# Kernel tuning notes

Measured on AMD Instinct MI355X. Metric: run time of the kernel, lower is better.

Reference implementation:

```python
import jax, jax.numpy as jnp
import numpy as np

B, N, D, F, L, R = 16, 1024, 256, 128, 2, 2


def setup_inputs() -> dict:
    key = jax.random.key(0)
    ks = jax.random.split(key, 12)
    s = 0.05
    return {
        "node_embed": jax.random.normal(ks[0], (B, N, D), jnp.float32),
        "input_x": jax.random.normal(ks[1], (B, F), jnp.float32),
        "adj": jax.random.randint(ks[2], (R, B, N, N), 0, 2, jnp.int32),
        "WQi_w": jax.random.normal(ks[3], (L, F, F), jnp.float32) * s,
        "WQi_b": jnp.zeros((L, F), jnp.float32),
        "WQ_w": jax.random.normal(ks[4], (L, D + F, D), jnp.float32) * s,
        "WQ_b": jnp.zeros((L, D), jnp.float32),
        "WK_w": jax.random.normal(ks[5], (L, R, D + F, D), jnp.float32) * s,
        "WK_b": jnp.zeros((L, R, D), jnp.float32),
        "WV_w": jax.random.normal(ks[6], (L, R, D + F, D), jnp.float32) * s,
        "WV_b": jnp.zeros((L, R, D), jnp.float32),
        "WF_w": jax.random.normal(ks[7], (L, R * D, D), jnp.float32) * s,
        "WF_b": jnp.zeros((L, D), jnp.float32),
        "ln_g": jnp.ones((L, D), jnp.float32),
        "ln_b": jnp.zeros((L, D), jnp.float32),
    }


def _layer_norm(x, g, b, eps=1e-5):
    mu = jnp.mean(x, axis=-1, keepdims=True)
    var = jnp.var(x, axis=-1, keepdims=True)
    return (x - mu) * jax.lax.rsqrt(var + eps) * g + b


def reference(node_embed, input_x, adj, WQi_w, WQi_b, WQ_w, WQ_b,
              WK_w, WK_b, WV_w, WV_b, WF_w, WF_b, ln_g, ln_b):
    scale = 1.0 / (D ** 0.5)
    h = node_embed
    for l in range(L):
        # input feature projection, broadcast over nodes
        x1 = input_x @ WQi_w[l] + WQi_b[l]              # (B, F)
        x1 = jnp.broadcast_to(x1[:, None, :], (h.shape[0], h.shape[1], F))
        qc = jnp.concatenate([h, x1], axis=-1)          # (B, N, D+F)
        q = qc @ WQ_w[l] + WQ_b[l]                      # (B, N, D)
        outs = []
        for r in range(R):
            k = qc @ WK_w[l, r] + WK_b[l, r]            # (B, N, D)
            v = qc @ WV_w[l, r] + WV_b[l, r]            # (B, N, D)
            scores = jnp.einsum('bnd,bmd->bnm', q, k) * scale
            scores = jnp.where(adj[r] == 0, -1e9, scores)
            alpha = jax.nn.softmax(scores, axis=-1)
            outs.append(jnp.einsum('bnm,bmd->bnd', alpha, v))
        h_concat = jnp.concatenate(outs, axis=-1)       # (B, N, R*D)
        h_fused = jax.nn.relu(h_concat @ WF_w[l] + WF_b[l])
        h = _layer_norm(h + h_fused, ln_g[l], ln_b[l])
    return h
```

## Files before the change

### kernel.cpp

```cpp
#include <hip/hip_runtime.h>
#include <hip/hip_bf16.h>

#define BB 16
#define NN 1024
#define DD 256
#define FF_ 128
#define LL 2
#define RR 2
#define DF 384
#define MM (BB*NN)
#define NPROJ 1280
#define PK 768

typedef __attribute__((ext_vector_type(8))) short s16x8;
typedef __attribute__((ext_vector_type(4))) float f32x4;
typedef __attribute__((ext_vector_type(16))) float f32x16;
typedef __attribute__((ext_vector_type(4))) unsigned int u32x4;
typedef __attribute__((ext_vector_type(4))) unsigned short us16x4;

__device__ __forceinline__ unsigned short f2bf(float f){
  unsigned u = __builtin_bit_cast(unsigned, f);
  u += 0x7fff + ((u >> 16) & 1);
  return (unsigned short)(u >> 16);
}

__device__ __forceinline__ void gload16(const void* g, void* l){
  __builtin_amdgcn_global_load_lds(
      (const __attribute__((address_space(1))) unsigned int*)g,
      (__attribute__((address_space(3))) unsigned int*)l, 16, 0, 0);
}

#define MFMA16(a,b,c) __builtin_amdgcn_mfma_f32_16x16x32_bf16((a),(b),(c),0,0,0)
#define MFMA32(a,b,c) __builtin_amdgcn_mfma_f32_32x32x16_bf16((a),(b),(c),0,0,0)

__global__ __launch_bounds__(256) void pack_adj(const int* __restrict__ adj,
                                                unsigned long long* __restrict__ bits){
  int w = threadIdx.x >> 6, lane = threadIdx.x & 63;
  size_t row = (size_t)blockIdx.x * 4 + w;
  const int* a = adj + row * NN;
  unsigned long long* brow = bits + row * 16;
  #pragma unroll
  for (int j = 0; j < 16; ++j){
    unsigned long long m = __ballot(a[j*64 + lane] != 0);
    if (lane == 0) brow[j] = m;
  }
}

#define PREP_WT   3840
#define PREP_WTF  1024
#define PREP_BALL 10
#define PREP_X1   16
#define PREP_H    2048
#define PREP_TOT  (PREP_WT+PREP_WTF+PREP_BALL+PREP_X1+PREP_H)

__global__ __launch_bounds__(256) void prep(
    const float* __restrict__ node, const float* __restrict__ inx,
    const float* __restrict__ WQi_w, const float* __restrict__ WQi_b,
    const float* __restrict__ WQ_w, const float* __restrict__ WK_w,
    const float* __restrict__ WV_w, const float* __restrict__ WQ_b,
    const float* __restrict__ WK_b, const float* __restrict__ WV_b,
    const float* __restrict__ WF_w,
    unsigned short* __restrict__ wtall, unsigned short* __restrict__ wtf,
    float* __restrict__ ball, unsigned short* __restrict__ x1bf,
    unsigned short* __restrict__ hbf){
  int bid = blockIdx.x, t = threadIdx.x;
  if (bid < PREP_WT){
    int o = bid*256 + t;
    int l = o / (NPROJ*DF); int oo = o - l*(NPROJ*DF);
    int n = oo / DF, k = oo - n*DF;
    const float* WQ = WQ_w + (size_t)l*DF*256;
    const float* WK = WK_w + (size_t)l*RR*DF*256;
    const float* WV = WV_w + (size_t)l*RR*DF*256;
    float v;
    if (n < 256)      v = WQ[(size_t)k*256 + n];
    else if (n < 768) v = WK[(size_t)((n-256)>>8)*(DF*256) + (size_t)k*256 + ((n-256)&255)];
    else              v = WV[(size_t)((n-768)>>8)*(DF*256) + (size_t)k*256 + ((n-768)&255)];
    wtall[o] = f2bf(v);
  } else if (bid < PREP_WT + PREP_WTF){
    int o = (bid - PREP_WT)*256 + t;
    int l = o >> 17; int oo = o & 131071;
    int n = oo >> 9, k = oo & 511;
    wtf[o] = f2bf(WF_w[(size_t)l*512*256 + (size_t)k*256 + n]);
  } else if (bid < PREP_WT + PREP_WTF + PREP_BALL){
    int o = (bid - PREP_WT - PREP_WTF)*256 + t;
    if (o < 2*NPROJ){
      int l = o / NPROJ, n = o - l*NPROJ;
      float v = (n < 256) ? WQ_b[l*256 + n]
              : (n < 768) ? WK_b[(size_t)l*512 + (n-256)]
                          : WV_b[(size_t)l*512 + (n-768)];
      ball[o] = v;
    }
  } else if (bid < PREP_WT + PREP_WTF + PREP_BALL + PREP_X1){
    int o = (bid - PREP_WT - PREP_WTF - PREP_BALL)*256 + t;
    int l = o >> 11, bj = o & 2047;
    int b = bj >> 7, j = bj & 127;
    const float* w = WQi_w + (size_t)l*FF_*FF_;
    float s = WQi_b[l*FF_ + j];
    for (int i = 0; i < FF_; ++i) s += inx[b*FF_ + i] * w[i*FF_ + j];
    x1bf[o] = f2bf(s);
  } else {
    int o = (bid - (PREP_TOT - PREP_H))*256 + t;
    const float4* src = (const float4*)node + (size_t)o*2;
    float4 a = src[0], c = src[1];
    uint4 pk;
    pk.x = (unsigned)f2bf(a.x) | ((unsigned)f2bf(a.y) << 16);
    pk.y = (unsigned)f2bf(a.z) | ((unsigned)f2bf(a.w) << 16);
    pk.z = (unsigned)f2bf(c.x) | ((unsigned)f2bf(c.y) << 16);
    pk.w = (unsigned)f2bf(c.z) | ((unsigned)f2bf(c.w) << 16);
    *(uint4*)(hbf + (size_t)o*8) = pk;
  }
}

__global__ __launch_bounds__(256) void gemm_big(const unsigned short* __restrict__ hbf,
    const unsigned short* __restrict__ x1l, const unsigned short* __restrict__ Wt,
    const float* __restrict__ bias, unsigned short* __restrict__ POUT,
    unsigned short* __restrict__ vtall){
  __shared__ unsigned short As[2][128*32];
  __shared__ unsigned short Bs[2][128*32];
  int t = threadIdx.x, lane = t & 63, w = t >> 6;
  int wr = w >> 1, wc = w & 1, l15 = lane & 15, lhi = lane >> 4;
  int bm = blockIdx.x, bn = blockIdx.y, bb = bm >> 3;
  f32x4 acc[4][4];
  #pragma unroll
  for (int m = 0; m < 4; ++m)
    #pragma unroll
    for (int n = 0; n < 4; ++n) acc[m][n] = (f32x4){0.f,0.f,0.f,0.f};

  auto STAGE = [&](int bi, int kk){
    #pragma unroll
    for (int i = 0; i < 2; ++i){
      int base = w*2048 + i*1024;
      int off = base + lane*16;
      int row = off >> 6, cb = off & 63;
      const char* asrc = (kk < 8)
        ? (const char*)hbf + ((size_t)(bm*128 + row)*256 + kk*32)*2 + cb
        : (const char*)x1l + ((size_t)bb*128 + (kk-8)*32)*2 + cb;
      gload16(asrc, (char*)As[bi] + base);
      gload16((const char*)Wt + ((size_t)(bn*128 + row)*DF + kk*32)*2 + cb,
              (char*)Bs[bi] + base);
    }
  };

  STAGE(0, 0);
  __syncthreads();
  for (int kk = 0; kk < 12; ++kk){
    int cur = kk & 1;
    if (kk + 1 < 12) STAGE(cur ^ 1, kk + 1);
    s16x8 af[4], bfr[4];
    #pragma unroll
    for (int m = 0; m < 4; ++m) af[m]  = *(const s16x8*)&As[cur][(wr*64 + m*16 + l15)*32 + lhi*8];
    #pragma unroll
    for (int n = 0; n < 4; ++n) bfr[n] = *(const s16x8*)&Bs[cur][(wc*64 + n*16 + l15)*32 + lhi*8];
    __builtin_amdgcn_s_setprio(1);
    #pragma unroll
    for (int m = 0; m < 4; ++m)
      #pragma unroll
      for (int n = 0; n < 4; ++n)
        acc[m][n] = MFMA16(af[m], bfr[n], acc[m][n]);
    __builtin_amdgcn_s_setprio(0);
    __syncthreads();
  }

  if (bn < 6){
    #pragma unroll
    for (int n = 0; n < 4; ++n){
      int gn = bn*128 + wc*64 + n*16 + l15;
      float bv = bias[gn];
      #pragma unroll
      for (int m = 0; m < 4; ++m){
        int gm = bm*128 + wr*64 + m*16 + lhi*4;
        #pragma unroll
        for (int i = 0; i < 4; ++i)
          POUT[(size_t)(gm + i)*PK + gn] = f2bf(acc[m][n][i] + bv);
      }
    }
  } else {
    #pragma unroll
    for (int n = 0; n < 4; ++n){
      int gn = bn*128 + wc*64 + n*16 + l15;
      float bv = bias[gn];
      int rv = gn - 768;
      int r = rv >> 8, d = rv & 255;
      #pragma unroll
      for (int m = 0; m < 4; ++m){
        int mb = (bm & 7)*128 + wr*64 + m*16 + lhi*4;
        us16x4 pk;
        #pragma unroll
        for (int i = 0; i < 4; ++i) pk[i] = f2bf(acc[m][n][i] + bv);
        *(us16x4*)(vtall + ((size_t)((r*16 + bb)*256 + d))*NN + mb) = pk;
      }
    }
  }
}

__global__ __launch_bounds__(512, 2) void attn4(const unsigned short* __restrict__ P,
    const unsigned short* __restrict__ VT, const unsigned long long* __restrict__ bits,
    unsigned short* __restrict__ hc){
  __shared__ unsigned short Kt[64*256];
  __shared__ unsigned short Vt[256*64];
  int t = threadIdx.x, lane = t & 63, w = t >> 6;
  int h = lane >> 5, l31 = lane & 31;
  int qsub = w >> 1, dh = w & 1;
  int F = blockIdx.x;
  int xcd = F & 7, j = F >> 3;
  int qt = j & 7;
  int gidx = xcd*4 + (j >> 3);
  int b = gidx & 15, r = gidx >> 4;
  const float C = 0.09016844f;

  size_t kcol = 256 + (size_t)r*256;
  const unsigned short* Vb = VT + ((size_t)(r*16 + b))*256*NN;

  int qrow = qt*128 + qsub*32 + l31;
  s16x8 qf[16];
  {
    const unsigned short* qp = P + ((size_t)(b*NN + qrow))*PK + h*8;
    #pragma unroll
    for (int d_ = 0; d_ < 16; ++d_) qf[d_] = *(const s16x8*)(qp + d_*16);
  }

  f32x16 acc[4];
  #pragma unroll
  for (int dt = 0; dt < 4; ++dt)
    #pragma unroll
    for (int i = 0; i < 16; ++i) acc[dt][i] = 0.f;
  float mrow = -3e38f, lrow = 0.f;
  const unsigned long long* bitp = bits + ((size_t)(r*BB + b)*NN + qrow)*16;

  for (int kt = 0; kt < 16; ++kt){
    __syncthreads();
    #pragma unroll
    for (int i = 0; i < 4; ++i){
      int base = w*4096 + i*1024;
      int off = base + lane*16;
      int row = off >> 9, cb = off & 511;
      int scb = cb ^ ((row & 7) << 4);
      gload16((const char*)P + ((size_t)(b*NN + kt*64 + row)*PK + kcol)*2 + scb,
              (char*)Kt + base);
    }
    #pragma unroll
    for (int i = 0; i < 4; ++i){
      int base = w*4096 + i*1024;
      int off = base + lane*16;
      int row = off >> 7, cb = off & 127;
      int scb = cb ^ ((row & 7) << 4);
      gload16((const char*)Vb + ((size_t)row*NN + kt*64)*2 + scb,
              (char*)Vt + base);
    }
    __syncthreads();

    f32x16 st[2];
    #pragma unroll
    for (int s = 0; s < 2; ++s){
      #pragma unroll
      for (int i = 0; i < 16; ++i) st[s][i] = 0.f;
      int krow = s*32 + l31;
      int swz = (krow & 7) << 4;
      #pragma unroll
      for (int d_ = 0; d_ < 16; ++d_){
        s16x8 kf = *(const s16x8*)((const char*)Kt + krow*512 + ((d_*32 + h*16) ^ swz));
        st[s] = MFMA32(kf, qf[d_], st[s]);
      }
    }

    unsigned long long mwv = bitp[kt];
    float ev[2][16];
    float tm = -3e38f;
    #pragma unroll
    for (int s = 0; s < 2; ++s)
      #pragma unroll
      for (int rr = 0; rr < 16; ++rr){
        int kb = s*32 + (rr & 3) + 8*(rr >> 2) + 4*h;
        float sval = st[s][rr] * C;
        sval = ((mwv >> kb) & 1ULL) ? sval : -1.443e9f;
        ev[s][rr] = sval;
        tm = fmaxf(tm, sval);
      }
    tm = fmaxf(tm, __shfl_xor(tm, 32));
    bool need = tm > mrow + 11.6f;
    if (__any(need)){
      float f = need ? exp2f(mrow - tm) : 1.f;
      if (need) mrow = tm;
      lrow *= f;
      #pragma unroll
      for (int rr = 0; rr < 16; ++rr){
        float fr = __shfl(f, (rr & 3) + 8*(rr >> 2) + 4*h);
        acc[0][rr] *= fr; acc[1][rr] *= fr; acc[2][rr] *= fr; acc[3][rr] *= fr;
      }
    }
    float rs = 0.f;
    #pragma unroll
    for (int s = 0; s < 2; ++s)
      #pragma unroll
      for (int rr = 0; rr < 16; ++rr){
        float e = exp2f(ev[s][rr] - mrow);
        ev[s][rr] = e;
        rs += e;
      }
    rs += __shfl_xor(rs, 32);
    lrow += rs;

    unsigned Pm[2][4][2];
    #pragma unroll
    for (int s = 0; s < 2; ++s)
      #pragma unroll
      for (int m = 0; m < 4; ++m)
        #pragma unroll
        for (int c = 0; c < 2; ++c)
          Pm[s][m][c] = (unsigned)f2bf(ev[s][4*m + 2*c])
                      | ((unsigned)f2bf(ev[s][4*m + 2*c + 1]) << 16);

    s16x8 pa[4];
    #pragma unroll
    for (int ks = 0; ks < 4; ++ks){
      const int s = ks >> 1, idx = ks & 1;
      unsigned own0 = h ? Pm[s][2*idx+1][0] : Pm[s][2*idx][0];
      unsigned own1 = h ? Pm[s][2*idx+1][1] : Pm[s][2*idx][1];
      unsigned snd0 = h ? Pm[s][2*idx][0]   : Pm[s][2*idx+1][0];
      unsigned snd1 = h ? Pm[s][2*idx][1]   : Pm[s][2*idx+1][1];
      unsigned rx0 = (unsigned)__shfl_xor((int)snd0, 32);
      unsigned rx1 = (unsigned)__shfl_xor((int)snd1, 32);
      u32x4 pv;
      pv[0] = h ? rx0 : own0;
      pv[1] = h ? rx1 : own1;
      pv[2] = h ? own0 : rx0;
      pv[3] = h ? own1 : rx1;
      pa[ks] = __builtin_bit_cast(s16x8, pv);
    }

    #pragma unroll
    for (int dt = 0; dt < 4; ++dt){
      int vrow = dh*128 + dt*32 + l31;
      int swz = (vrow & 7) << 4;
      #pragma unroll
      for (int ks = 0; ks < 4; ++ks){
        s16x8 vf = *(const s16x8*)((const char*)Vt + vrow*128 + ((ks*32 + h*16) ^ swz));
        acc[dt] = MFMA32(pa[ks], vf, acc[dt]);
      }
    }
  }

  float linv = 1.f / lrow;
  #pragma unroll
  for (int rr = 0; rr < 16; ++rr){
    int rowo = (rr & 3) + 8*(rr >> 2) + 4*h;
    float ir = __shfl(linv, rowo);
    int q = qt*128 + qsub*32 + rowo;
    unsigned short* hrow = hc + ((size_t)(b*NN + q))*(RR*DD) + r*DD + dh*128 + l31;
    #pragma unroll
    for (int dt = 0; dt < 4; ++dt)
      hrow[dt*32] = f2bf(acc[dt][rr] * ir);
  }
}

__global__ __launch_bounds__(256) void gemm_ff(const unsigned short* __restrict__ A,
    const unsigned short* __restrict__ Wt, const float* __restrict__ bias,
    float* __restrict__ out){
  __shared__ unsigned short As[2][128*32];
  __shared__ unsigned short Bs[2][128*32];
  int t = threadIdx.x, lane = t & 63, w = t >> 6;
  int wr = w >> 1, wc = w & 1, l15 = lane & 15, lhi = lane >> 4;
  int bm = blockIdx.x, bn = blockIdx.y;
  f32x4 acc[4][4];
  #pragma unroll
  for (int m = 0; m < 4; ++m)
    #pragma unroll
    for (int n = 0; n < 4; ++n) acc[m][n] = (f32x4){0.f,0.f,0.f,0.f};

  auto STAGE = [&](int bi, int kk){
    #pragma unroll
    for (int i = 0; i < 2; ++i){
      int base = w*2048 + i*1024;
      int off = base + lane*16;
      int row = off >> 6, cb = off & 63;
      gload16((const char*)A  + ((size_t)(bm*128 + row)*512 + kk*32)*2 + cb,
              (char*)As[bi] + base);
      gload16((const char*)Wt + ((size_t)(bn*128 + row)*512 + kk*32)*2 + cb,
              (char*)Bs[bi] + base);
    }
  };

  STAGE(0, 0);
  __syncthreads();
  for (int kk = 0; kk < 16; ++kk){
    int cur = kk & 1;
    if (kk + 1 < 16) STAGE(cur ^ 1, kk + 1);
    s16x8 af[4], bfr[4];
    #pragma unroll
    for (int m = 0; m < 4; ++m) af[m]  = *(const s16x8*)&As[cur][(wr*64 + m*16 + l15)*32 + lhi*8];
    #pragma unroll
    for (int n = 0; n < 4; ++n) bfr[n] = *(const s16x8*)&Bs[cur][(wc*64 + n*16 + l15)*32 + lhi*8];
    __builtin_amdgcn_s_setprio(1);
    #pragma unroll
    for (int m = 0; m < 4; ++m)
      #pragma unroll
      for (int n = 0; n < 4; ++n)
        acc[m][n] = MFMA16(af[m], bfr[n], acc[m][n]);
    __builtin_amdgcn_s_setprio(0);
    __syncthreads();
  }

  #pragma unroll
  for (int n = 0; n < 4; ++n){
    int gn = bn*128 + wc*64 + n*16 + l15;
    float bv = bias[gn];
    #pragma unroll
    for (int m = 0; m < 4; ++m){
      int gm = bm*128 + wr*64 + m*16 + lhi*4;
      #pragma unroll
      for (int i = 0; i < 4; ++i)
        out[(size_t)(gm + i)*DD + gn] = acc[m][n][i] + bv;
    }
  }
}

template<int WRITEH>
__global__ __launch_bounds__(256) void ln_res2(const float* __restrict__ ff,
    const float* __restrict__ hin, const float* __restrict__ g,
    const float* __restrict__ bv, float* __restrict__ hout,
    unsigned short* __restrict__ hbf){
  int w = threadIdx.x >> 6, lane = threadIdx.x & 63;
  size_t row = (size_t)blockIdx.x * 4 + w;
  f32x4 fv = *(const f32x4*)(ff  + row*DD + lane*4);
  f32x4 hv = *(const f32x4*)(hin + row*DD + lane*4);
  float x[4], s = 0.f, ss = 0.f;
  #pragma unroll
  for (int j = 0; j < 4; ++j){ x[j] = fmaxf(fv[j], 0.f) + hv[j]; s += x[j]; ss += x[j]*x[j]; }
  #pragma unroll
  for (int xm = 1; xm < 64; xm <<= 1){ s += __shfl_xor(s, xm); ss += __shfl_xor(ss, xm); }
  float mu = s * (1.f/256.f);
  float var = ss * (1.f/256.f) - mu*mu;
  float rstd = rsqrtf(var + 1e-5f);
  f32x4 o;
  #pragma unroll
  for (int j = 0; j < 4; ++j){ int c = lane*4 + j; o[j] = (x[j]-mu)*rstd*g[c] + bv[c]; }
  *(f32x4*)(hout + row*DD + lane*4) = o;
  if (WRITEH){
    uint2 pv;
    pv.x = (unsigned)f2bf(o[0]) | ((unsigned)f2bf(o[1]) << 16);
    pv.y = (unsigned)f2bf(o[2]) | ((unsigned)f2bf(o[3]) << 16);
    *(uint2*)(hbf + row*DD + lane*4) = pv;
  }
}

extern "C" void kernel_launch(void* const* d_in, const int* in_sizes, int n_in,
                              void* d_out, int out_size, void* d_ws, size_t ws_size,
                              hipStream_t stream){
  (void)in_sizes; (void)n_in; (void)out_size; (void)ws_size;
  const float* node  = (const float*)d_in[0];
  const float* inx   = (const float*)d_in[1];
  const int*   adj   = (const int*)d_in[2];
  const float* WQi_w = (const float*)d_in[3];
  const float* WQi_b = (const float*)d_in[4];
  const float* WQ_w  = (const float*)d_in[5];
  const float* WQ_b  = (const float*)d_in[6];
  const float* WK_w  = (const float*)d_in[7];
  const float* WK_b  = (const float*)d_in[8];
  const float* WV_w  = (const float*)d_in[9];
  const float* WV_b  = (const float*)d_in[10];
  const float* WF_w  = (const float*)d_in[11];
  const float* WF_b  = (const float*)d_in[12];
  const float* ln_g  = (const float*)d_in[13];
  const float* ln_b  = (const float*)d_in[14];
  float* hout = (float*)d_out;

  char* wsp = (char*)d_ws;
  auto alloc = [&](size_t n){ char* p = wsp; wsp += (n + 255) & ~(size_t)255; return p; };
  unsigned long long* bits = (unsigned long long*)alloc((size_t)RR*BB*NN*16*8);
  unsigned short* wtall = (unsigned short*)alloc((size_t)2*NPROJ*DF*2);
  unsigned short* wtf   = (unsigned short*)alloc((size_t)2*DD*512*2);
  float*          ball  = (float*)alloc((size_t)2*NPROJ*4);
  unsigned short* x1bf  = (unsigned short*)alloc((size_t)2*BB*FF_*2);
  unsigned short* hbf   = (unsigned short*)alloc((size_t)MM*DD*2);
  unsigned short* POUT  = (unsigned short*)alloc((size_t)MM*PK*2);
  unsigned short* vtall = (unsigned short*)alloc((size_t)RR*BB*DD*NN*2);
  unsigned short* hc    = (unsigned short*)alloc((size_t)MM*512*2);
  float*          ffo   = (float*)alloc((size_t)MM*DD*4);

  pack_adj<<<RR*BB*NN/4, 256, 0, stream>>>(adj, bits);
  prep<<<PREP_TOT, 256, 0, stream>>>(node, inx, WQi_w, WQi_b, WQ_w, WK_w, WV_w,
                                     WQ_b, WK_b, WV_b, WF_w,
                                     wtall, wtf, ball, x1bf, hbf);

  for (int l = 0; l < LL; ++l){
    gemm_big<<<dim3(128,10), 256, 0, stream>>>(hbf, x1bf + (size_t)l*BB*FF_,
        wtall + (size_t)l*NPROJ*DF, ball + (size_t)l*NPROJ, POUT, vtall);

    attn4<<<256, 512, 0, stream>>>(POUT, vtall, bits, hc);

    gemm_ff<<<dim3(128,2), 256, 0, stream>>>(hc, wtf + (size_t)l*DD*512, WF_b + l*DD, ffo);

    if (l == 0) ln_res2<1><<<MM/4, 256, 0, stream>>>(ffo, node, ln_g, ln_b, hout, hbf);
    else        ln_res2<0><<<MM/4, 256, 0, stream>>>(ffo, (const float*)hout,
                                                     ln_g + DD, ln_b + DD, hout, nullptr);
  }
}
```

Before: 325.9 us.

## Rework attention kernel with double-buffered K/V tiles and full-D waves

Replaces attn4 with attn5, which uses 256 threads where each wave handles 32 query rows across the full 256-wide head dimension, so P@V needs no split across waves. K/V tiles are double-buffered in 128KB of LDS with async global-to-LDS loads, and the next tile is prefetched while the current one is computed. Softmax now runs per 32-key half, using hardware bf16 pack conversion and a per-thread rescale instead of shuffles. Output is staged through LDS so stores to global memory are coalesced. The cost is one block per CU and more accumulator registers (8 f32x16 per lane), which lowers occupancy.

```diff
diff --git a/kernel.cpp b/kernel.cpp
--- a/kernel.cpp
+++ b/kernel.cpp
@@ -15,6 +15,7 @@
 typedef __attribute__((ext_vector_type(8))) short s16x8;
 typedef __attribute__((ext_vector_type(4))) float f32x4;
 typedef __attribute__((ext_vector_type(16))) float f32x16;
+typedef __attribute__((ext_vector_type(2))) unsigned int u32x2;
 typedef __attribute__((ext_vector_type(4))) unsigned int u32x4;
 typedef __attribute__((ext_vector_type(4))) unsigned short us16x4;
 
@@ -193,14 +194,13 @@
   }
 }
 
-__global__ __launch_bounds__(512, 2) void attn4(const unsigned short* __restrict__ P,
+__global__ __launch_bounds__(256, 1) void attn5(const unsigned short* __restrict__ P,
     const unsigned short* __restrict__ VT, const unsigned long long* __restrict__ bits,
     unsigned short* __restrict__ hc){
-  __shared__ unsigned short Kt[64*256];
-  __shared__ unsigned short Vt[256*64];
+  __shared__ char smem[131072];
+
   int t = threadIdx.x, lane = t & 63, w = t >> 6;
   int h = lane >> 5, l31 = lane & 31;
-  int qsub = w >> 1, dh = w & 1;
   int F = blockIdx.x;
   int xcd = F & 7, j = F >> 3;
   int qt = j & 7;
@@ -211,7 +211,8 @@
   size_t kcol = 256 + (size_t)r*256;
   const unsigned short* Vb = VT + ((size_t)(r*16 + b))*256*NN;
 
-  int qrow = qt*128 + qsub*32 + l31;
+  int qrow = qt*128 + w*32 + l31;
+
   s16x8 qf[16];
   {
     const unsigned short* qp = P + ((size_t)(b*NN + qrow))*PK + h*8;
@@ -219,137 +220,161 @@
     for (int d_ = 0; d_ < 16; ++d_) qf[d_] = *(const s16x8*)(qp + d_*16);
   }
 
-  f32x16 acc[4];
-  #pragma unroll
-  for (int dt = 0; dt < 4; ++dt)
+  f32x16 acc[8];
+  #pragma unroll
+  for (int dt = 0; dt < 8; ++dt)
     #pragma unroll
     for (int i = 0; i < 16; ++i) acc[dt][i] = 0.f;
   float mrow = -3e38f, lrow = 0.f;
   const unsigned long long* bitp = bits + ((size_t)(r*BB + b)*NN + qrow)*16;
 
-  for (int kt = 0; kt < 16; ++kt){
-    __syncthreads();
-    #pragma unroll
-    for (int i = 0; i < 4; ++i){
-      int base = w*4096 + i*1024;
+  auto STAGE = [&](int bi, int kt){
+    char* Kd = smem + bi*32768;
+    char* Vd = smem + 65536 + bi*32768;
+    #pragma unroll
+    for (int i = 0; i < 8; ++i){
+      int base = w*8192 + i*1024;
       int off = base + lane*16;
       int row = off >> 9, cb = off & 511;
       int scb = cb ^ ((row & 7) << 4);
       gload16((const char*)P + ((size_t)(b*NN + kt*64 + row)*PK + kcol)*2 + scb,
-              (char*)Kt + base);
-    }
-    #pragma unroll
-    for (int i = 0; i < 4; ++i){
-      int base = w*4096 + i*1024;
+              Kd + base);
+    }
+    #pragma unroll
+    for (int i = 0; i < 8; ++i){
+      int base = w*8192 + i*1024;
       int off = base + lane*16;
       int row = off >> 7, cb = off & 127;
       int scb = cb ^ ((row & 7) << 4);
       gload16((const char*)Vb + ((size_t)row*NN + kt*64)*2 + scb,
-              (char*)Vt + base);
-    }
-    __syncthreads();
-
-    f32x16 st[2];
+              Vd + base);
+    }
+  };
+
+  STAGE(0, 0);
+
+  for (int kt = 0; kt < 16; ++kt){
+    __builtin_amdgcn_s_barrier();
+    unsigned long long mwv = bitp[kt];
+    if (kt + 1 < 16){
+      STAGE((kt+1)&1, kt+1);
+      asm volatile("s_waitcnt vmcnt(16)" ::: "memory");
+    } else {
+      asm volatile("s_waitcnt vmcnt(0)" ::: "memory");
+    }
+    __builtin_amdgcn_s_barrier();
+    __builtin_amdgcn_sched_barrier(0);
+
+    const char* Kcur = smem + (kt & 1)*32768;
+    const char* Vcur = smem + 65536 + (kt & 1)*32768;
+
     #pragma unroll
     for (int s = 0; s < 2; ++s){
-      #pragma unroll
-      for (int i = 0; i < 16; ++i) st[s][i] = 0.f;
+      f32x16 st;
+      #pragma unroll
+      for (int i = 0; i < 16; ++i) st[i] = 0.f;
       int krow = s*32 + l31;
-      int swz = (krow & 7) << 4;
+      int swzk = (krow & 7) << 4;
+      const char* kbase = Kcur + krow*512;
       #pragma unroll
       for (int d_ = 0; d_ < 16; ++d_){
-        s16x8 kf = *(const s16x8*)((const char*)Kt + krow*512 + ((d_*32 + h*16) ^ swz));
-        st[s] = MFMA32(kf, qf[d_], st[s]);
-      }
-    }
-
-    unsigned long long mwv = bitp[kt];
-    float ev[2][16];
-    float tm = -3e38f;
-    #pragma unroll
-    for (int s = 0; s < 2; ++s)
+        s16x8 kf = *(const s16x8*)(kbase + ((d_*32 + h*16) ^ swzk));
+        st = MFMA32(kf, qf[d_], st);
+      }
+
+      unsigned mw = (unsigned)(mwv >> (s*32));
+      float tm = -3e38f;
       #pragma unroll
       for (int rr = 0; rr < 16; ++rr){
-        int kb = s*32 + (rr & 3) + 8*(rr >> 2) + 4*h;
-        float sval = st[s][rr] * C;
-        sval = ((mwv >> kb) & 1ULL) ? sval : -1.443e9f;
-        ev[s][rr] = sval;
-        tm = fmaxf(tm, sval);
-      }
-    tm = fmaxf(tm, __shfl_xor(tm, 32));
-    bool need = tm > mrow + 11.6f;
-    if (__any(need)){
-      float f = need ? exp2f(mrow - tm) : 1.f;
-      if (need) mrow = tm;
-      lrow *= f;
+        int kb = (rr & 3) + 8*(rr >> 2) + 4*h;
+        float sv = st[rr] * C;
+        sv = ((mw >> kb) & 1u) ? sv : -1.443e9f;
+        st[rr] = sv;
+        tm = fmaxf(tm, sv);
+      }
+      tm = fmaxf(tm, __shfl_xor(tm, 32));
+      if (tm > mrow + 10.f){
+        float f = exp2f(mrow - tm);
+        mrow = tm;
+        lrow *= f;
+        #pragma unroll
+        for (int dt = 0; dt < 8; ++dt)
+          #pragma unroll
+          for (int i = 0; i < 16; ++i) acc[dt][i] *= f;
+      }
+      float rs = 0.f;
       #pragma unroll
       for (int rr = 0; rr < 16; ++rr){
-        float fr = __shfl(f, (rr & 3) + 8*(rr >> 2) + 4*h);
-        acc[0][rr] *= fr; acc[1][rr] *= fr; acc[2][rr] *= fr; acc[3][rr] *= fr;
-      }
-    }
-    float rs = 0.f;
-    #pragma unroll
-    for (int s = 0; s < 2; ++s)
-      #pragma unroll
-      for (int rr = 0; rr < 16; ++rr){
-        float e = exp2f(ev[s][rr] - mrow);
-        ev[s][rr] = e;
+        float e = exp2f(st[rr] - mrow);
+        st[rr] = e;
         rs += e;
       }
-    rs += __shfl_xor(rs, 32);
-    lrow += rs;
-
-    unsigned Pm[2][4][2];
-    #pragma unroll
-    for (int s = 0; s < 2; ++s)
-      #pragma unroll
-      for (int m = 0; m < 4; ++m)
-        #pragma unroll
-        for (int c = 0; c < 2; ++c)
-          Pm[s][m][c] = (unsigned)f2bf(ev[s][4*m + 2*c])
-                      | ((unsigned)f2bf(ev[s][4*m + 2*c + 1]) << 16);
-
-    s16x8 pa[4];
-    #pragma unroll
-    for (int ks = 0; ks < 4; ++ks){
-      const int s = ks >> 1, idx = ks & 1;
-      unsigned own0 = h ? Pm[s][2*idx+1][0] : Pm[s][2*idx][0];
-      unsigned own1 = h ? Pm[s][2*idx+1][1] : Pm[s][2*idx][1];
-      unsigned snd0 = h ? Pm[s][2*idx][0]   : Pm[s][2*idx+1][0];
-      unsigned snd1 = h ? Pm[s][2*idx][1]   : Pm[s][2*idx+1][1];
-      unsigned rx0 = (unsigned)__shfl_xor((int)snd0, 32);
-      unsigned rx1 = (unsigned)__shfl_xor((int)snd1, 32);
-      u32x4 pv;
-      pv[0] = h ? rx0 : own0;
-      pv[1] = h ? rx1 : own1;
-      pv[2] = h ? own0 : rx0;
-      pv[3] = h ? own1 : rx1;
-      pa[ks] = __builtin_bit_cast(s16x8, pv);
-    }
-
-    #pragma unroll
-    for (int dt = 0; dt < 4; ++dt){
-      int vrow = dh*128 + dt*32 + l31;
-      int swz = (vrow & 7) << 4;
-      #pragma unroll
-      for (int ks = 0; ks < 4; ++ks){
-        s16x8 vf = *(const s16x8*)((const char*)Vt + vrow*128 + ((ks*32 + h*16) ^ swz));
-        acc[dt] = MFMA32(pa[ks], vf, acc[dt]);
-      }
-    }
-  }
-
-  float linv = 1.f / lrow;
-  #pragma unroll
-  for (int rr = 0; rr < 16; ++rr){
-    int rowo = (rr & 3) + 8*(rr >> 2) + 4*h;
-    float ir = __shfl(linv, rowo);
-    int q = qt*128 + qsub*32 + rowo;
-    unsigned short* hrow = hc + ((size_t)(b*NN + q))*(RR*DD) + r*DD + dh*128 + l31;
-    #pragma unroll
-    for (int dt = 0; dt < 4; ++dt)
-      hrow[dt*32] = f2bf(acc[dt][rr] * ir);
+      rs += __shfl_xor(rs, 32);
+      lrow += rs;
+
+      unsigned pk[8];
+      #pragma unroll
+      for (int p = 0; p < 8; ++p){
+        unsigned rpk;
+        float lo = st[p*2], hi = st[p*2+1];
+        asm("v_cvt_pk_bf16_f32 %0, %1, %2" : "=v"(rpk) : "v"(lo), "v"(hi));
+        pk[p] = rpk;
+      }
+      unsigned sA = h ? pk[0] : pk[2], sB = h ? pk[1] : pk[3];
+      unsigned sC = h ? pk[4] : pk[6], sD = h ? pk[5] : pk[7];
+      unsigned rxA = (unsigned)__shfl_xor((int)sA, 32);
+      unsigned rxB = (unsigned)__shfl_xor((int)sB, 32);
+      unsigned rxC = (unsigned)__shfl_xor((int)sC, 32);
+      unsigned rxD = (unsigned)__shfl_xor((int)sD, 32);
+      u32x4 pv0, pv1;
+      pv0[0] = h ? rxA : pk[0]; pv0[1] = h ? rxB : pk[1];
+      pv0[2] = h ? pk[2] : rxA; pv0[3] = h ? pk[3] : rxB;
+      pv1[0] = h ? rxC : pk[4]; pv1[1] = h ? rxD : pk[5];
+      pv1[2] = h ? pk[6] : rxC; pv1[3] = h ? pk[7] : rxD;
+      s16x8 pa0 = __builtin_bit_cast(s16x8, pv0);
+      s16x8 pa1 = __builtin_bit_cast(s16x8, pv1);
+
+      #pragma unroll
+      for (int dt = 0; dt < 8; ++dt){
+        int vrow = dt*32 + l31;
+        int swzv = (vrow & 7) << 4;
+        const char* vbase = Vcur + vrow*128;
+        s16x8 vf0 = *(const s16x8*)(vbase + (((2*s)*32 + h*16) ^ swzv));
+        acc[dt] = MFMA32(vf0, pa0, acc[dt]);
+        s16x8 vf1 = *(const s16x8*)(vbase + (((2*s+1)*32 + h*16) ^ swzv));
+        acc[dt] = MFMA32(vf1, pa1, acc[dt]);
+      }
+    }
+  }
+
+  __builtin_amdgcn_s_barrier();
+  float inv = 1.f / lrow;
+  unsigned short* Ob = (unsigned short*)smem;
+  int qloc = w*32 + l31;
+  #pragma unroll
+  for (int dt = 0; dt < 8; ++dt){
+    #pragma unroll
+    for (int g = 0; g < 4; ++g){
+      float a0 = acc[dt][g*4+0]*inv, a1 = acc[dt][g*4+1]*inv;
+      float a2 = acc[dt][g*4+2]*inv, a3 = acc[dt][g*4+3]*inv;
+      unsigned r0, r1;
+      asm("v_cvt_pk_bf16_f32 %0, %1, %2" : "=v"(r0) : "v"(a0), "v"(a1));
+      asm("v_cvt_pk_bf16_f32 %0, %1, %2" : "=v"(r1) : "v"(a2), "v"(a3));
+      int d = dt*32 + 8*g + 4*h;
+      int byteoff = qloc*512 + ((d*2) ^ ((qloc & 7) << 4));
+      u32x2 pv; pv[0] = r0; pv[1] = r1;
+      *(u32x2*)((char*)Ob + byteoff) = pv;
+    }
+  }
+  __builtin_amdgcn_s_barrier();
+  #pragma unroll
+  for (int it = 0; it < 16; ++it){
+    int off = (it*256 + t) * 16;
+    int row = off >> 9, cb = off & 511;
+    int scb = cb ^ ((row & 7) << 4);
+    u32x4 v = *(const u32x4*)((char*)Ob + row*512 + scb);
+    int q = qt*128 + row;
+    *(u32x4*)((char*)hc + (((size_t)(b*NN + q))*512 + r*256 + (cb >> 1))*2) = v;
   }
 }
 
@@ -486,7 +511,7 @@
     gemm_big<<<dim3(128,10), 256, 0, stream>>>(hbf, x1bf + (size_t)l*BB*FF_,
         wtall + (size_t)l*NPROJ*DF, ball + (size_t)l*NPROJ, POUT, vtall);
 
-    attn4<<<256, 512, 0, stream>>>(POUT, vtall, bits, hc);
+    attn5<<<256, 256, 0, stream>>>(POUT, vtall, bits, hc);
 
     gemm_ff<<<dim3(128,2), 256, 0, stream>>>(hc, wtf + (size_t)l*DD*512, WF_b + l*DD, ffo);
 
```

New measurement: 303.0 us. -7.0%, faster.
